# Performance work log

Hardware: AMD Instinct MI355X
Metric: run time of the kernel (lower is better)

Reference implementation:

```python
import math
import jax, jax.numpy as jnp
import numpy as np

K_MODES = 8
L_ITERS = 8
ALPHA_INIT = 2000.0
TAU_INIT = 0.01


def setup_inputs() -> dict:
    key = jax.random.key(0)
    B, T, C = 64, 4096, 16
    x = jax.random.normal(key, (B, T, C), dtype=jnp.float32)
    log_alpha = jnp.full((L_ITERS, K_MODES), math.log(ALPHA_INIT), dtype=jnp.float32)
    raw_tau = jnp.full((L_ITERS,), math.log(math.expm1(TAU_INIT) + 1e-08), dtype=jnp.float32)
    omega_init = np.linspace(0.05, 0.45, K_MODES)
    raw_omega = jnp.asarray(np.log(2.0 * omega_init / (1.0 - 2.0 * omega_init + 1e-08)), dtype=jnp.float32)
    return {"x": x, "log_alpha": log_alpha, "raw_tau": raw_tau, "raw_omega": raw_omega}


def reference(x, log_alpha, raw_tau, raw_omega):
    B, T, C = x.shape
    L, K = log_alpha.shape
    T_rfft = T // 2 + 1

    alpha = jnp.exp(log_alpha)                    # (L, K)
    tau = jax.nn.softplus(raw_tau)                # (L,)
    omega = jax.nn.sigmoid(raw_omega) * 0.5       # (K,)

    freqs = jnp.linspace(0.0, 0.5, T_rfft, dtype=x.dtype)  # (T_rfft,)
    # (B, T, C) -> (B*C, T)
    x_bc = jnp.transpose(x, (0, 2, 1)).reshape(B * C, T)
    f_hat = jnp.fft.rfft(x_bc, axis=-1)           # (B*C, T_rfft) complex

    # Precompute all denominators: (L, K, T_rfft)
    denom = 1.0 + 2.0 * alpha[:, :, None] * (freqs[None, None, :] - omega[None, :, None]) ** 2

    u0 = jnp.zeros((B * C, K, T_rfft), dtype=f_hat.dtype)
    lam0 = jnp.zeros_like(f_hat)

    def step(carry, per_layer):
        u, lam = carry
        den_l, tau_l = per_layer
        u_sum = u.sum(axis=1)  # (B*C, T_rfft)
        # Jacobi update for all K modes simultaneously
        numerator = f_hat[:, None, :] - (u_sum[:, None, :] - u) + 0.5 * lam[:, None, :]
        u_new = numerator / den_l[None, :, :]
        lam_new = lam + tau_l * (f_hat - u_new.sum(axis=1))
        return (u_new, lam_new), None

    (u_final, _), _ = jax.lax.scan(step, (u0, lam0), (denom, tau))

    modes_flat = jnp.fft.irfft(u_final, n=T, axis=-1)  # (B*C, K, T)
    modes = jnp.transpose(modes_flat.reshape(B, C, K, T), (0, 2, 3, 1))  # (B, K, T, C)
    return modes
```

## Files before the change

kernel.cpp:

```cpp
#include <hip/hip_runtime.h>
#include <math.h>

#ifndef M_PI
#define M_PI 3.14159265358979323846
#endif

#define T_LEN 4096
#define M_LEN 2048
#define NFREQ 2049
#define KM 8
#define LI 8
#define CD 16

__device__ __forceinline__ float2 cadd(float2 a, float2 b){ return make_float2(a.x+b.x, a.y+b.y); }
__device__ __forceinline__ float2 csub(float2 a, float2 b){ return make_float2(a.x-b.x, a.y-b.y); }
__device__ __forceinline__ float2 cmul(float2 a, float2 b){ return make_float2(a.x*b.x - a.y*b.y, a.x*b.y + a.y*b.x); }
__device__ __forceinline__ float2 muli(float2 a){ return make_float2(-a.y, a.x); }
#define RC 0.70710678118654752440f
__device__ __forceinline__ float2 mulw81(float2 a){ return make_float2(RC*(a.x-a.y), RC*(a.x+a.y)); }
__device__ __forceinline__ float2 mulw83(float2 a){ return make_float2(-RC*(a.x+a.y), RC*(a.x-a.y)); }

#define SWZ(i) ((i) ^ (((i) >> 4) & 15))

__device__ __forceinline__ void dft8_inv(const float2 a[8], float2 x[8]) {
    float2 s0=cadd(a[0],a[4]), s1=cadd(a[1],a[5]), s2=cadd(a[2],a[6]), s3=cadd(a[3],a[7]);
    float2 d0=csub(a[0],a[4]), d1=csub(a[1],a[5]), d2=csub(a[2],a[6]), d3=csub(a[3],a[7]);
    d1 = mulw81(d1); d2 = muli(d2); d3 = mulw83(d3);
    float2 e0=cadd(s0,s2), e2=csub(s0,s2), e1=cadd(s1,s3), e3=muli(csub(s1,s3));
    float2 f0=cadd(d0,d2), f2=csub(d0,d2), f1=cadd(d1,d3), f3=muli(csub(d1,d3));
    x[0]=cadd(e0,e1); x[4]=csub(e0,e1); x[2]=cadd(e2,e3); x[6]=csub(e2,e3);
    x[1]=cadd(f0,f1); x[5]=csub(f0,f1); x[3]=cadd(f2,f3); x[7]=csub(f2,f3);
}

template<int MSTAGE>
__device__ __forceinline__ void r8_stage(float2* S, int lt) {
    float2 a[8];
    #pragma unroll
    for (int k = 0; k < 8; ++k) a[k] = S[SWZ(lt + 256*k)];
    __syncthreads();
    float2 x[8];
    dft8_inv(a, x);
    const int j = lt / MSTAGE;
    const int r = lt % MSTAGE;
    float th = ((float)M_PI / 1024.0f) * (float)(j * MSTAGE);
    float swv, cwv; __sincosf(th, &swv, &cwv);
    float2 w1 = make_float2(cwv, swv);
    float2 w2 = cmul(w1,w1), w3 = cmul(w2,w1), w4 = cmul(w2,w2);
    float2 w5 = cmul(w3,w2), w6 = cmul(w3,w3), w7 = cmul(w4,w3);
    x[1]=cmul(x[1],w1); x[2]=cmul(x[2],w2); x[3]=cmul(x[3],w3);
    x[4]=cmul(x[4],w4); x[5]=cmul(x[5],w5); x[6]=cmul(x[6],w6); x[7]=cmul(x[7],w7);
    const int base = r + 8*MSTAGE*j;
    #pragma unroll
    for (int k = 0; k < 8; ++k) S[SWZ(base + MSTAGE*k)] = x[k];
    __syncthreads();
}

__device__ __forceinline__ void r4_stage_pair(float2* S, int lt) {
    float2 b[2][4];
    #pragma unroll
    for (int h = 0; h < 2; ++h) {
        int i2 = lt + 256*h;
        #pragma unroll
        for (int k = 0; k < 4; ++k) b[h][k] = S[SWZ(i2 + 512*k)];
    }
    __syncthreads();
    #pragma unroll
    for (int h = 0; h < 2; ++h) {
        int i2 = lt + 256*h;
        float2 s02=cadd(b[h][0],b[h][2]), d02=csub(b[h][0],b[h][2]);
        float2 s13=cadd(b[h][1],b[h][3]), d13=muli(csub(b[h][1],b[h][3]));
        S[SWZ(i2 +    0)] = cadd(s02,s13);
        S[SWZ(i2 +  512)] = cadd(d02,d13);
        S[SWZ(i2 + 1024)] = csub(s02,s13);
        S[SWZ(i2 + 1536)] = csub(d02,d13);
    }
    __syncthreads();
}

template <int NT>
__device__ __forceinline__ float2* fft2048(float2* a, float2* b, int tid, float sign) {
    float2* src = a;
    float2* dst = b;
    int l = 1024;
    #pragma unroll 1
    for (int s = 0; s < 11; ++s) {
        float piol = sign * (float)M_PI / (float)l;
        #pragma unroll
        for (int ii = 0; ii < 1024 / NT; ++ii) {
            int i = tid + ii * NT;
            int j = i >> s;
            float2 A = src[i];
            float2 B = src[i + 1024];
            float ang = piol * (float)j;
            float sw, cw;
            __sincosf(ang, &sw, &cw);
            float2 sum = make_float2(A.x + B.x, A.y + B.y);
            float2 dif = make_float2(A.x - B.x, A.y - B.y);
            float2 tw = make_float2(dif.x * cw - dif.y * sw, dif.x * sw + dif.y * cw);
            int p = i + (j << s);
            dst[p] = sum;
            dst[p + (1 << s)] = tw;
        }
        __syncthreads();
        float2* t = src; src = dst; dst = t;
        l >>= 1;
    }
    return src;
}

__global__ void __launch_bounds__(512)
k_fwd_iter(const float* __restrict__ x,
           const float* __restrict__ log_alpha,
           const float* __restrict__ raw_tau,
           const float* __restrict__ raw_omega,
           float2* __restrict__ u_ws)
{
    __shared__ float2 bufA[M_LEN];
    __shared__ float2 bufB[M_LEN];
    __shared__ float s_2a[LI * KM];
    __shared__ float s_tau[LI];
    __shared__ float s_om[KM];

    const int tid = threadIdx.x;
    const int row = blockIdx.x;
    const int b = row >> 4;
    const int c = row & 15;

    if (tid < LI * KM) s_2a[tid] = 2.0f * __expf(log_alpha[tid]);
    if (tid < LI)      s_tau[tid] = log1pf(__expf(raw_tau[tid]));
    if (tid < KM)      s_om[tid]  = 0.5f / (1.0f + __expf(-raw_omega[tid]));

    const float* xr = x + (size_t)b * T_LEN * CD + c;
    #pragma unroll
    for (int q = 0; q < 4; ++q) {
        int n = tid + q * 512;
        float e = xr[(size_t)(2 * n) * CD];
        float o = xr[(size_t)(2 * n + 1) * CD];
        bufA[n] = make_float2(e, o);
    }
    __syncthreads();

    float2* Z = fft2048<512>(bufA, bufB, tid, -1.0f);

    const size_t sb = (size_t)(b * (KM * CD) + c);

    for (int f = tid; f < NFREQ; f += 512) {
        float2 Zk = Z[f & (M_LEN - 1)];
        float2 Zm = Z[(M_LEN - f) & (M_LEN - 1)];
        float2 E = make_float2(0.5f * (Zk.x + Zm.x), 0.5f * (Zk.y - Zm.y));
        float2 D = make_float2(0.5f * (Zk.x - Zm.x), 0.5f * (Zk.y + Zm.y));
        float2 O = make_float2(D.y, -D.x);
        float ang = -2.0f * (float)M_PI * (float)f / (float)T_LEN;
        float sw, cw;
        __sincosf(ang, &sw, &cw);
        float fhx = E.x + cw * O.x - sw * O.y;
        float fhy = E.y + cw * O.y + sw * O.x;

        float freq = (float)f * (0.5f / (float)M_LEN);
        float dd[KM];
        #pragma unroll
        for (int k = 0; k < KM; ++k) {
            float d = freq - s_om[k];
            dd[k] = d * d;
        }

        float2 u[KM];
        #pragma unroll
        for (int k = 0; k < KM; ++k) u[k] = make_float2(0.f, 0.f);
        float lamx = 0.f, lamy = 0.f;

        #pragma unroll
        for (int l = 0; l < LI; ++l) {
            float usx = 0.f, usy = 0.f;
            #pragma unroll
            for (int k = 0; k < KM; ++k) { usx += u[k].x; usy += u[k].y; }
            float bx = fhx - usx + 0.5f * lamx;
            float by = fhy - usy + 0.5f * lamy;
            float sx = 0.f, sy = 0.f;
            #pragma unroll
            for (int k = 0; k < KM; ++k) {
                float den = fmaf(s_2a[l * KM + k], dd[k], 1.0f);
                float r = __builtin_amdgcn_rcpf(den);
                float ux = (bx + u[k].x) * r;
                float uy = (by + u[k].y) * r;
                u[k].x = ux; u[k].y = uy;
                sx += ux; sy += uy;
            }
            lamx += s_tau[l] * (fhx - sx);
            lamy += s_tau[l] * (fhy - sy);
        }

        #pragma unroll
        for (int k = 0; k < KM; ++k) {
            u_ws[(sb + (size_t)k * CD) * NFREQ + f] = u[k];
        }
    }
}

__global__ void __launch_bounds__(1024)
k_inv(const float2* __restrict__ u_ws, float* __restrict__ out)
{
    __shared__ float2 S[4][M_LEN];

    const int tid = threadIdx.x;
    const int g   = tid >> 8;
    const int lt  = tid & 255;
    const int bk  = blockIdx.x;

    float val[CD][4];
    const float sc = 1.0f / (float)M_LEN;

    #pragma unroll
    for (int cp = 0; cp < 4; ++cp) {
        const int c0 = 4 * cp;
        const float2* sp = u_ws + (size_t)(bk * CD + c0 + g) * NFREQ;

        #pragma unroll
        for (int q = 0; q < 4; ++q) {
            int j = lt + 256 * q;
            float2 Xj = sp[j];
            float2 Xm = sp[M_LEN - j];
            float Ex = 0.5f * (Xj.x + Xm.x), Ey = 0.5f * (Xj.y - Xm.y);
            float Dx = 0.5f * (Xj.x - Xm.x), Dy = 0.5f * (Xj.y + Xm.y);
            float ang = (2.0f * (float)M_PI / (float)T_LEN) * (float)j;
            float swv, cwv;
            __sincosf(ang, &swv, &cwv);
            float Ox = cwv * Dx - swv * Dy;
            float Oy = cwv * Dy + swv * Dx;
            S[g][SWZ(j)] = make_float2((Ex - Oy) * sc, (Ey + Ox) * sc);
            if (j > 0) {
                S[g][SWZ(M_LEN - j)] = make_float2((Ex + Oy) * sc, (Ox - Ey) * sc);
            } else {
                float2 Xq = sp[1024];
                S[g][SWZ(1024)] = make_float2(Xq.x * sc, -Xq.y * sc);
            }
        }
        __syncthreads();

        r8_stage<1>(S[g], lt);
        r8_stage<8>(S[g], lt);
        r8_stage<64>(S[g], lt);
        r4_stage_pair(S[g], lt);

        #pragma unroll
        for (int cc = 0; cc < 4; ++cc) {
            float2 z0 = S[cc][SWZ(2 * tid)];
            float2 z1 = S[cc][SWZ(2 * tid + 1)];
            val[c0 + cc][0] = z0.x;
            val[c0 + cc][1] = z0.y;
            val[c0 + cc][2] = z1.x;
            val[c0 + cc][3] = z1.y;
        }
        __syncthreads();
    }

    float4* op = (float4*)(out + ((size_t)bk * T_LEN + (size_t)(4 * tid)) * CD);
    #pragma unroll
    for (int r = 0; r < 4; ++r) {
        #pragma unroll
        for (int g2 = 0; g2 < 4; ++g2) {
            op[r * 4 + g2] = make_float4(val[4 * g2 + 0][r], val[4 * g2 + 1][r],
                                         val[4 * g2 + 2][r], val[4 * g2 + 3][r]);
        }
    }
}

extern "C" void kernel_launch(void* const* d_in, const int* in_sizes, int n_in,
                              void* d_out, int out_size, void* d_ws, size_t ws_size,
                              hipStream_t stream) {
    const float* x         = (const float*)d_in[0];
    const float* log_alpha = (const float*)d_in[1];
    const float* raw_tau   = (const float*)d_in[2];
    const float* raw_omega = (const float*)d_in[3];
    float* out = (float*)d_out;
    float2* u_ws = (float2*)d_ws;

    k_fwd_iter<<<dim3(64 * CD), dim3(512), 0, stream>>>(x, log_alpha, raw_tau,
                                                        raw_omega, u_ws);
    k_inv<<<dim3(64 * KM), dim3(1024), 0, stream>>>(u_ws, out);
}
```

Before: 414.8 us.

## Use radix-8 Stockham FFT in forward kernel, stage inverse input through LDS

Replaces the 11-stage radix-2 forward FFT with the templated radix-8/radix-4 pipeline already used for the inverse, with the sign as a template parameter. Each forward block now processes two rows with 256 threads each. The inverse kernel loads spectra coalesced into shared memory before the real-to-complex post-processing, instead of doing strided global reads of mirrored indices. It also writes output per channel group inside the loop rather than holding all values in registers. These changes cut forward-FFT barriers and sincos work and lower register pressure in the inverse, at the cost of an extra LDS pass and synchronisation.

New measurement: 470.0 us. 13.3% more time.

```diff
diff --git a/kernel.cpp b/kernel.cpp
--- a/kernel.cpp
+++ b/kernel.cpp
@@ -15,34 +15,47 @@
 __device__ __forceinline__ float2 cadd(float2 a, float2 b){ return make_float2(a.x+b.x, a.y+b.y); }
 __device__ __forceinline__ float2 csub(float2 a, float2 b){ return make_float2(a.x-b.x, a.y-b.y); }
 __device__ __forceinline__ float2 cmul(float2 a, float2 b){ return make_float2(a.x*b.x - a.y*b.y, a.x*b.y + a.y*b.x); }
-__device__ __forceinline__ float2 muli(float2 a){ return make_float2(-a.y, a.x); }
 #define RC 0.70710678118654752440f
-__device__ __forceinline__ float2 mulw81(float2 a){ return make_float2(RC*(a.x-a.y), RC*(a.x+a.y)); }
-__device__ __forceinline__ float2 mulw83(float2 a){ return make_float2(-RC*(a.x+a.y), RC*(a.x-a.y)); }
+
+template<int SGN>
+__device__ __forceinline__ float2 muli_s(float2 a){
+    return (SGN > 0) ? make_float2(-a.y, a.x) : make_float2(a.y, -a.x);
+}
+template<int SGN>
+__device__ __forceinline__ float2 w81_s(float2 a){
+    return (SGN > 0) ? make_float2(RC*(a.x-a.y), RC*(a.x+a.y))
+                     : make_float2(RC*(a.x+a.y), RC*(a.y-a.x));
+}
+template<int SGN>
+__device__ __forceinline__ float2 w83_s(float2 a){
+    return (SGN > 0) ? make_float2(-RC*(a.x+a.y), RC*(a.x-a.y))
+                     : make_float2(RC*(a.y-a.x), -RC*(a.x+a.y));
+}
 
 #define SWZ(i) ((i) ^ (((i) >> 4) & 15))
 
-__device__ __forceinline__ void dft8_inv(const float2 a[8], float2 x[8]) {
+template<int SGN>
+__device__ __forceinline__ void dft8_s(const float2 a[8], float2 x[8]) {
     float2 s0=cadd(a[0],a[4]), s1=cadd(a[1],a[5]), s2=cadd(a[2],a[6]), s3=cadd(a[3],a[7]);
     float2 d0=csub(a[0],a[4]), d1=csub(a[1],a[5]), d2=csub(a[2],a[6]), d3=csub(a[3],a[7]);
-    d1 = mulw81(d1); d2 = muli(d2); d3 = mulw83(d3);
-    float2 e0=cadd(s0,s2), e2=csub(s0,s2), e1=cadd(s1,s3), e3=muli(csub(s1,s3));
-    float2 f0=cadd(d0,d2), f2=csub(d0,d2), f1=cadd(d1,d3), f3=muli(csub(d1,d3));
+    d1 = w81_s<SGN>(d1); d2 = muli_s<SGN>(d2); d3 = w83_s<SGN>(d3);
+    float2 e0=cadd(s0,s2), e2=csub(s0,s2), e1=cadd(s1,s3), e3=muli_s<SGN>(csub(s1,s3));
+    float2 f0=cadd(d0,d2), f2=csub(d0,d2), f1=cadd(d1,d3), f3=muli_s<SGN>(csub(d1,d3));
     x[0]=cadd(e0,e1); x[4]=csub(e0,e1); x[2]=cadd(e2,e3); x[6]=csub(e2,e3);
     x[1]=cadd(f0,f1); x[5]=csub(f0,f1); x[3]=cadd(f2,f3); x[7]=csub(f2,f3);
 }
 
-template<int MSTAGE>
+template<int MSTAGE, int SGN>
 __device__ __forceinline__ void r8_stage(float2* S, int lt) {
     float2 a[8];
     #pragma unroll
     for (int k = 0; k < 8; ++k) a[k] = S[SWZ(lt + 256*k)];
     __syncthreads();
     float2 x[8];
-    dft8_inv(a, x);
+    dft8_s<SGN>(a, x);
     const int j = lt / MSTAGE;
     const int r = lt % MSTAGE;
-    float th = ((float)M_PI / 1024.0f) * (float)(j * MSTAGE);
+    float th = (float)SGN * ((float)M_PI / 1024.0f) * (float)(j * MSTAGE);
     float swv, cwv; __sincosf(th, &swv, &cwv);
     float2 w1 = make_float2(cwv, swv);
     float2 w2 = cmul(w1,w1), w3 = cmul(w2,w1), w4 = cmul(w2,w2);
@@ -55,6 +68,7 @@
     __syncthreads();
 }
 
+template<int SGN>
 __device__ __forceinline__ void r4_stage_pair(float2* S, int lt) {
     float2 b[2][4];
     #pragma unroll
@@ -68,44 +82,13 @@
     for (int h = 0; h < 2; ++h) {
         int i2 = lt + 256*h;
         float2 s02=cadd(b[h][0],b[h][2]), d02=csub(b[h][0],b[h][2]);
-        float2 s13=cadd(b[h][1],b[h][3]), d13=muli(csub(b[h][1],b[h][3]));
+        float2 s13=cadd(b[h][1],b[h][3]), d13=muli_s<SGN>(csub(b[h][1],b[h][3]));
         S[SWZ(i2 +    0)] = cadd(s02,s13);
         S[SWZ(i2 +  512)] = cadd(d02,d13);
         S[SWZ(i2 + 1024)] = csub(s02,s13);
         S[SWZ(i2 + 1536)] = csub(d02,d13);
     }
     __syncthreads();
-}
-
-template <int NT>
-__device__ __forceinline__ float2* fft2048(float2* a, float2* b, int tid, float sign) {
-    float2* src = a;
-    float2* dst = b;
-    int l = 1024;
-    #pragma unroll 1
-    for (int s = 0; s < 11; ++s) {
-        float piol = sign * (float)M_PI / (float)l;
-        #pragma unroll
-        for (int ii = 0; ii < 1024 / NT; ++ii) {
-            int i = tid + ii * NT;
-            int j = i >> s;
-            float2 A = src[i];
-            float2 B = src[i + 1024];
-            float ang = piol * (float)j;
-            float sw, cw;
-            __sincosf(ang, &sw, &cw);
-            float2 sum = make_float2(A.x + B.x, A.y + B.y);
-            float2 dif = make_float2(A.x - B.x, A.y - B.y);
-            float2 tw = make_float2(dif.x * cw - dif.y * sw, dif.x * sw + dif.y * cw);
-            int p = i + (j << s);
-            dst[p] = sum;
-            dst[p + (1 << s)] = tw;
-        }
-        __syncthreads();
-        float2* t = src; src = dst; dst = t;
-        l >>= 1;
-    }
-    return src;
 }
 
 __global__ void __launch_bounds__(512)
@@ -115,14 +98,15 @@
            const float* __restrict__ raw_omega,
            float2* __restrict__ u_ws)
 {
-    __shared__ float2 bufA[M_LEN];
-    __shared__ float2 bufB[M_LEN];
+    __shared__ float2 S[2][M_LEN];
     __shared__ float s_2a[LI * KM];
     __shared__ float s_tau[LI];
     __shared__ float s_om[KM];
 
     const int tid = threadIdx.x;
-    const int row = blockIdx.x;
+    const int g   = tid >> 8;
+    const int lt  = tid & 255;
+    const int row = blockIdx.x * 2 + g;
     const int b = row >> 4;
     const int c = row & 15;
 
@@ -132,21 +116,24 @@
 
     const float* xr = x + (size_t)b * T_LEN * CD + c;
     #pragma unroll
-    for (int q = 0; q < 4; ++q) {
-        int n = tid + q * 512;
+    for (int q = 0; q < 8; ++q) {
+        int n = lt + 256 * q;
         float e = xr[(size_t)(2 * n) * CD];
         float o = xr[(size_t)(2 * n + 1) * CD];
-        bufA[n] = make_float2(e, o);
-    }
-    __syncthreads();
-
-    float2* Z = fft2048<512>(bufA, bufB, tid, -1.0f);
+        S[g][SWZ(n)] = make_float2(e, o);
+    }
+    __syncthreads();
+
+    r8_stage<1,  -1>(S[g], lt);
+    r8_stage<8,  -1>(S[g], lt);
+    r8_stage<64, -1>(S[g], lt);
+    r4_stage_pair<-1>(S[g], lt);
 
     const size_t sb = (size_t)(b * (KM * CD) + c);
 
-    for (int f = tid; f < NFREQ; f += 512) {
-        float2 Zk = Z[f & (M_LEN - 1)];
-        float2 Zm = Z[(M_LEN - f) & (M_LEN - 1)];
+    for (int f = lt; f < NFREQ; f += 256) {
+        float2 Zk = S[g][SWZ(f & (M_LEN - 1))];
+        float2 Zm = S[g][SWZ((M_LEN - f) & (M_LEN - 1))];
         float2 E = make_float2(0.5f * (Zk.x + Zm.x), 0.5f * (Zk.y - Zm.y));
         float2 D = make_float2(0.5f * (Zk.x - Zm.x), 0.5f * (Zk.y + Zm.y));
         float2 O = make_float2(D.y, -D.x);
@@ -207,19 +194,25 @@
     const int lt  = tid & 255;
     const int bk  = blockIdx.x;
 
-    float val[CD][4];
     const float sc = 1.0f / (float)M_LEN;
-
-    #pragma unroll
+    float4* op = (float4*)(out + ((size_t)bk * T_LEN + (size_t)(4 * tid)) * CD);
+
+    #pragma unroll 1
     for (int cp = 0; cp < 4; ++cp) {
-        const int c0 = 4 * cp;
-        const float2* sp = u_ws + (size_t)(bk * CD + c0 + g) * NFREQ;
+        const float2* sp = u_ws + (size_t)(bk * CD + 4 * cp + g) * NFREQ;
+
+        #pragma unroll
+        for (int q = 0; q < 8; ++q) {
+            int n = lt + 256 * q;
+            S[g][SWZ(n)] = sp[n];
+        }
+        __syncthreads();
 
         #pragma unroll
         for (int q = 0; q < 4; ++q) {
             int j = lt + 256 * q;
-            float2 Xj = sp[j];
-            float2 Xm = sp[M_LEN - j];
+            float2 Xj = S[g][SWZ(j)];
+            float2 Xm = (j > 0) ? S[g][SWZ(M_LEN - j)] : sp[M_LEN];
             float Ex = 0.5f * (Xj.x + Xm.x), Ey = 0.5f * (Xj.y - Xm.y);
             float Dx = 0.5f * (Xj.x - Xm.x), Dy = 0.5f * (Xj.y + Xm.y);
             float ang = (2.0f * (float)M_PI / (float)T_LEN) * (float)j;
@@ -227,41 +220,37 @@
             __sincosf(ang, &swv, &cwv);
             float Ox = cwv * Dx - swv * Dy;
             float Oy = cwv * Dy + swv * Dx;
-            S[g][SWZ(j)] = make_float2((Ex - Oy) * sc, (Ey + Ox) * sc);
             if (j > 0) {
+                S[g][SWZ(j)]         = make_float2((Ex - Oy) * sc, (Ey + Ox) * sc);
                 S[g][SWZ(M_LEN - j)] = make_float2((Ex + Oy) * sc, (Ox - Ey) * sc);
             } else {
-                float2 Xq = sp[1024];
+                float2 Xq = S[g][SWZ(1024)];
+                S[g][SWZ(0)]    = make_float2((Ex - Oy) * sc, (Ey + Ox) * sc);
                 S[g][SWZ(1024)] = make_float2(Xq.x * sc, -Xq.y * sc);
             }
         }
         __syncthreads();
 
-        r8_stage<1>(S[g], lt);
-        r8_stage<8>(S[g], lt);
-        r8_stage<64>(S[g], lt);
-        r4_stage_pair(S[g], lt);
-
+        r8_stage<1,  1>(S[g], lt);
+        r8_stage<8,  1>(S[g], lt);
+        r8_stage<64, 1>(S[g], lt);
+        r4_stage_pair<1>(S[g], lt);
+
+        float v[4][4];
         #pragma unroll
         for (int cc = 0; cc < 4; ++cc) {
             float2 z0 = S[cc][SWZ(2 * tid)];
             float2 z1 = S[cc][SWZ(2 * tid + 1)];
-            val[c0 + cc][0] = z0.x;
-            val[c0 + cc][1] = z0.y;
-            val[c0 + cc][2] = z1.x;
-            val[c0 + cc][3] = z1.y;
+            v[cc][0] = z0.x;
+            v[cc][1] = z0.y;
+            v[cc][2] = z1.x;
+            v[cc][3] = z1.y;
+        }
+        #pragma unroll
+        for (int r = 0; r < 4; ++r) {
+            op[r * 4 + cp] = make_float4(v[0][r], v[1][r], v[2][r], v[3][r]);
         }
         __syncthreads();
-    }
-
-    float4* op = (float4*)(out + ((size_t)bk * T_LEN + (size_t)(4 * tid)) * CD);
-    #pragma unroll
-    for (int r = 0; r < 4; ++r) {
-        #pragma unroll
-        for (int g2 = 0; g2 < 4; ++g2) {
-            op[r * 4 + g2] = make_float4(val[4 * g2 + 0][r], val[4 * g2 + 1][r],
-                                         val[4 * g2 + 2][r], val[4 * g2 + 3][r]);
-        }
     }
 }
 
@@ -275,7 +264,7 @@
     float* out = (float*)d_out;
     float2* u_ws = (float2*)d_ws;
 
-    k_fwd_iter<<<dim3(64 * CD), dim3(512), 0, stream>>>(x, log_alpha, raw_tau,
-                                                        raw_omega, u_ws);
+    k_fwd_iter<<<dim3(64 * CD / 2), dim3(512), 0, stream>>>(x, log_alpha, raw_tau,
+                                                            raw_omega, u_ws);
     k_inv<<<dim3(64 * KM), dim3(1024), 0, stream>>>(u_ws, out);
 }
```
